# Performance work log

Hardware: AMD Instinct MI355X
Metric: run time of the kernel (lower is better)

## Reference

```python
import jax, jax.numpy as jnp
import numpy as np

HID = 64
NUM_LAYER = 3
N_OBJ = 100000
N_P1, N_P2, N_P3 = 200000, 400000, 200000
NUM_GRAPHS = 256


def _mlp(x, w1, b1, w2, b2):
    # pyg.nn.MLP([in, hid, out], norm=None): Linear -> ReLU -> Linear
    return jnp.dot(jax.nn.relu(jnp.dot(x, w1) + b1), w2) + b2


def _gather(obj, ei):
    # ei: [arity, n_atoms] object index per argument slot
    r, n = ei.shape
    g = jnp.take(obj, ei, axis=0)  # [r, n, HID]
    return jnp.moveaxis(g, 0, 1).reshape(n, r * HID)  # concat per-position embeddings


def _scatter(atom, ei, n_obj):
    # split atom embedding [n, r*HID] into r chunks and scatter-add to objects
    r, n = ei.shape
    chunks = jnp.moveaxis(atom.reshape(n, r, HID), 1, 0).reshape(r * n, HID)
    return jax.ops.segment_sum(chunks, ei.reshape(-1), num_segments=n_obj)


def _lin_init(key, fan_in, fan_out):
    kw, kb = jax.random.split(key)
    w = jax.random.normal(kw, (fan_in, fan_out), jnp.float32) / np.float32(np.sqrt(fan_in))
    b = jax.random.normal(kb, (fan_out,), jnp.float32) * 0.01
    return w, b


def setup_inputs() -> dict:
    key = jax.random.key(0)
    ks = jax.random.split(key, 16)
    inp = {}
    inp["x_obj"] = jnp.zeros((N_OBJ, 1), jnp.float32)
    inp["x_p1"] = jnp.zeros((N_P1, 1), jnp.float32)
    inp["x_p2"] = jnp.zeros((N_P2, 2), jnp.float32)
    inp["x_p3"] = jnp.zeros((N_P3, 3), jnp.float32)
    for i, (name, r) in enumerate([("p1", 1), ("p2", 2), ("p3", 3)]):
        d = HID * r
        w1, b1 = _lin_init(ks[2 * i], d, d)
        w2, b2 = _lin_init(ks[2 * i + 1], d, d)
        inp[f"w_{name}_1"], inp[f"b_{name}_1"] = w1, b1
        inp[f"w_{name}_2"], inp[f"b_{name}_2"] = w2, b2
    inp["w_u1"], inp["b_u1"] = _lin_init(ks[6], 2 * HID, 2 * HID)
    inp["w_u2"], inp["b_u2"] = _lin_init(ks[7], 2 * HID, HID)
    inp["w_r1"], inp["b_r1"] = _lin_init(ks[8], HID, 2 * HID)
    inp["w_r2"], inp["b_r2"] = _lin_init(ks[9], 2 * HID, 1)
    inp["ei_p1"] = jax.random.randint(ks[10], (1, N_P1), 0, N_OBJ, jnp.int32)
    inp["ei_p2"] = jax.random.randint(ks[11], (2, N_P2), 0, N_OBJ, jnp.int32)
    inp["ei_p3"] = jax.random.randint(ks[12], (3, N_P3), 0, N_OBJ, jnp.int32)
    inp["batch_obj"] = jnp.sort(jax.random.randint(ks[13], (N_OBJ,), 0, NUM_GRAPHS, jnp.int32))
    inp["num_graphs"] = NUM_GRAPHS
    return inp


def reference(x_obj, x_p1, x_p2, x_p3,
              w_p1_1, b_p1_1, w_p1_2, b_p1_2,
              w_p2_1, b_p2_1, w_p2_2, b_p2_2,
              w_p3_1, b_p3_1, w_p3_2, b_p3_2,
              w_u1, b_u1, w_u2, b_u2,
              w_r1, b_r1, w_r2, b_r2,
              ei_p1, ei_p2, ei_p3, batch_obj, num_graphs):
    n_obj = x_obj.shape[0]
    # encoding_layer: everything starts at zeros of size [N, F*hidden]
    obj = jnp.zeros((n_obj, x_obj.shape[1] * HID), jnp.float32)
    for _ in range(NUM_LAYER):
        # FanOutMP: gather arg-object embeddings, per-predicate MLP -> atom embeddings
        a1 = _mlp(_gather(obj, ei_p1), w_p1_1, b_p1_1, w_p1_2, b_p1_2)
        a2 = _mlp(_gather(obj, ei_p2), w_p2_1, b_p2_1, w_p2_2, b_p2_2)
        a3 = _mlp(_gather(obj, ei_p3), w_p3_1, b_p3_1, w_p3_2, b_p3_2)
        # FanInMP: split atom emb into arity chunks, scatter-add back to objects
        agg = (_scatter(a1, ei_p1, n_obj) + _scatter(a2, ei_p2, n_obj)
               + _scatter(a3, ei_p3, n_obj))
        # obj_update on cat([old_obj, aggregated])
        obj = _mlp(jnp.concatenate([obj, agg], axis=1), w_u1, b_u1, w_u2, b_u2)
    # global_add_pool + readout
    pooled = jax.ops.segment_sum(obj, batch_obj, num_segments=num_graphs)
    return _mlp(pooled, w_r1, b_r1, w_r2, b_r2).reshape(-1)
```

## Files before the change

### kernel.cpp

```cpp
#include <hip/hip_runtime.h>

typedef _Float16 h8 __attribute__((ext_vector_type(8)));
typedef _Float16 h4 __attribute__((ext_vector_type(4)));
typedef float f32x4 __attribute__((ext_vector_type(4)));

__device__ __forceinline__ f32x4 mfma2(h8 ah, h8 bh, h8 bl, f32x4 c) {
    c = __builtin_amdgcn_mfma_f32_16x16x32_f16(ah, bh, c, 0, 0, 0);
    c = __builtin_amdgcn_mfma_f32_16x16x32_f16(ah, bl, c, 0, 0, 0);
    return c;
}

__launch_bounds__(256)
__global__ void wprep(const float* __restrict__ w_p1_1, const float* __restrict__ w_p1_2,
                      const float* __restrict__ w_p2_1, const float* __restrict__ w_p2_2,
                      const float* __restrict__ w_p3_1, const float* __restrict__ w_p3_2,
                      const float* __restrict__ w_u1, const float* __restrict__ w_u2,
                      _Float16* __restrict__ hb)
{
    int b = blockIdx.x;
    const float* src; int K, N, base; size_t off;
    if      (b < 16)  { src = w_p1_1; K = 64;  N = 64;  base = 0;   off = 0;      }
    else if (b < 32)  { src = w_p1_2; K = 64;  N = 64;  base = 16;  off = 8192;   }
    else if (b < 96)  { src = w_p2_1; K = 128; N = 128; base = 32;  off = 16384;  }
    else if (b < 160) { src = w_p2_2; K = 128; N = 128; base = 96;  off = 49152;  }
    else if (b < 304) { src = w_p3_1; K = 192; N = 192; base = 160; off = 81920;  }
    else if (b < 448) { src = w_p3_2; K = 192; N = 192; base = 304; off = 155648; }
    else if (b < 512) { src = w_u1;   K = 128; N = 128; base = 448; off = 229376; }
    else              { src = w_u2;   K = 128; N = 64;  base = 512; off = 262144; }
    int e = (b - base) * 256 + threadIdx.x;
    if (e < K * N) {
        int n = e / K, k = e - n * K;
        float x = src[k * N + n];
        _Float16 h = (_Float16)x;
        hb[off + e] = h;
        hb[off + (size_t)K * N + e] = (_Float16)(x - (float)h);
    }
}

__launch_bounds__(256)
__global__ void aconst_k(const float* __restrict__ b_p1_1, const float* __restrict__ w_p1_2,
                         const float* __restrict__ b_p1_2,
                         const float* __restrict__ b_p2_1, const float* __restrict__ w_p2_2,
                         const float* __restrict__ b_p2_2,
                         const float* __restrict__ b_p3_1, const float* __restrict__ w_p3_2,
                         const float* __restrict__ b_p3_2,
                         float* __restrict__ ac)
{
    int p = blockIdx.x;
    const float *b1, *w2, *b2; int D, off;
    if      (p == 0) { b1 = b_p1_1; w2 = w_p1_2; b2 = b_p1_2; D = 64;  off = 0;   }
    else if (p == 1) { b1 = b_p2_1; w2 = w_p2_2; b2 = b_p2_2; D = 128; off = 64;  }
    else             { b1 = b_p3_1; w2 = w_p3_2; b2 = b_p3_2; D = 192; off = 192; }
    int n = threadIdx.x;
    if (n < D) {
        float s = b2[n];
        for (int k = 0; k < D; ++k) {
            float h = b1[k];
            h = h > 0.f ? h : 0.f;
            s = fmaf(h, w2[k * D + n], s);
        }
        ac[off + n] = s;
    }
}

__launch_bounds__(256)
__global__ void hist_k(const int* __restrict__ ei1, const int* __restrict__ ei2,
                       const int* __restrict__ ei3, int* __restrict__ counts,
                       int n_obj, int n1, int n2, int n3)
{
    int e = blockIdx.x * 256 + threadIdx.x;
    int t1 = n1, t2 = n1 + 2 * n2, t3 = t2 + 3 * n3;
    if (e < t1) {
        atomicAdd(&counts[ei1[e]], 1);
    } else if (e < t2) {
        int x = e - t1; int slot = x / n2;
        atomicAdd(&counts[(size_t)(1 + slot) * n_obj + ei2[x]], 1);
    } else if (e < t3) {
        int x = e - t2; int slot = x / n3;
        atomicAdd(&counts[(size_t)(3 + slot) * n_obj + ei3[x]], 1);
    }
}

__launch_bounds__(256)
__global__ void bcast_k(const int* __restrict__ counts, const float* __restrict__ ac,
                        float* __restrict__ agg, int n_obj)
{
    __shared__ float ch[384];
    int tid = threadIdx.x;
    for (int i = tid; i < 384; i += 256) ch[i] = ac[i];
    __syncthreads();
    int i = blockIdx.x * 256 + tid;
    int o = i >> 4, q = i & 15;
    if (o < n_obj) {
        float c[6];
#pragma unroll
        for (int j = 0; j < 6; ++j) c[j] = (float)counts[(size_t)j * n_obj + o];
        float4 v;
        float* vp = (float*)&v;
#pragma unroll
        for (int comp = 0; comp < 4; ++comp) {
            int col = 4 * q + comp;
            float s = 0.f;
#pragma unroll
            for (int j = 0; j < 6; ++j) s = fmaf(c[j], ch[j * 64 + col], s);
            vp[comp] = s;
        }
        ((float4*)agg)[(size_t)o * 16 + q] = v;
    }
}

template<int R>
__device__ __forceinline__ void pred_body(
    char* smem,
    const _Float16* __restrict__ objh, const int* __restrict__ ei,
    const _Float16* __restrict__ W1h, const _Float16* __restrict__ W1l,
    const float* __restrict__ B1,
    const _Float16* __restrict__ W2h, const _Float16* __restrict__ W2l,
    const float* __restrict__ B2,
    float* __restrict__ agg, int n_atoms, int blk)
{
    constexpr int D = 64 * R;
    constexpr int KC = D / 32;
    constexpr int LDA = D + 8;
    _Float16* Ah = (_Float16*)smem;
    int* eis = (int*)(Ah + 64 * LDA);

    const int tid = threadIdx.x;
    const int wave = tid >> 6, lane = tid & 63;
    const int r = lane & 15, g = lane >> 4;
    const int a_base = blk * 64;
    const int tb = wave * R;

    for (int i = tid; i < R * 64; i += 256) {
        int s = i >> 6, a = i & 63;
        int ag = a_base + a; if (ag >= n_atoms) ag = n_atoms - 1;
        eis[i] = ei[s * n_atoms + ag];
    }
    __syncthreads();
    {
        h8 vv[2 * R];
#pragma unroll
        for (int i = 0; i < 2 * R; ++i) {
            int f = tid + 256 * i;
            int rowslot = f >> 3, c = f & 7;
            int s = rowslot >> 6, a = rowslot & 63;
            vv[i] = *(const h8*)(objh + (size_t)eis[s * 64 + a] * 64 + c * 8);
        }
#pragma unroll
        for (int i = 0; i < 2 * R; ++i) {
            int f = tid + 256 * i;
            int rowslot = f >> 3, c = f & 7;
            int s = rowslot >> 6, a = rowslot & 63;
            *(h8*)(Ah + a * LDA + s * 64 + c * 8) = vv[i];
        }
    }
    __syncthreads();

    f32x4 z = {0.f, 0.f, 0.f, 0.f};
    f32x4 acc[4][R];
#pragma unroll
    for (int rt = 0; rt < 4; ++rt)
#pragma unroll
        for (int t = 0; t < R; ++t) acc[rt][t] = z;

    {
        h8 bh[2][R], bl[2][R];
#pragma unroll
        for (int t = 0; t < R; ++t) {
            size_t wo = (size_t)((tb + t) * 16 + r) * D + g * 8;
            bh[0][t] = *(const h8*)(W1h + wo);
            bl[0][t] = *(const h8*)(W1l + wo);
        }
#pragma unroll
        for (int kc = 0; kc < KC; ++kc) {
            const int cur = kc & 1, nxt = cur ^ 1;
            if (kc + 1 < KC) {
#pragma unroll
                for (int t = 0; t < R; ++t) {
                    size_t wo = (size_t)((tb + t) * 16 + r) * D + (kc + 1) * 32 + g * 8;
                    bh[nxt][t] = *(const h8*)(W1h + wo);
                    bl[nxt][t] = *(const h8*)(W1l + wo);
                }
            }
            const int ko = kc * 32 + g * 8;
            h8 ah[4];
#pragma unroll
            for (int rt = 0; rt < 4; ++rt)
                ah[rt] = *(const h8*)(Ah + (rt * 16 + r) * LDA + ko);
#pragma unroll
            for (int t = 0; t < R; ++t)
#pragma unroll
                for (int rt = 0; rt < 4; ++rt)
                    acc[rt][t] = mfma2(ah[rt], bh[cur][t], bl[cur][t], acc[rt][t]);
        }
    }
    __syncthreads();

#pragma unroll
    for (int t = 0; t < R; ++t) {
        int col = (tb + t) * 16 + r;
        float b1 = B1[col];
#pragma unroll
        for (int rt = 0; rt < 4; ++rt)
#pragma unroll
            for (int q = 0; q < 4; ++q) {
                int row = rt * 16 + g * 4 + q;
                float h = acc[rt][t][q] + b1;
                h = h > 0.f ? h : 0.f;
                Ah[row * LDA + col] = (_Float16)h;
            }
    }
    __syncthreads();

#pragma unroll
    for (int rt = 0; rt < 4; ++rt)
#pragma unroll
        for (int t = 0; t < R; ++t) acc[rt][t] = z;
    {
        h8 bh[2][R], bl[2][R];
#pragma unroll
        for (int t = 0; t < R; ++t) {
            size_t wo = (size_t)((tb + t) * 16 + r) * D + g * 8;
            bh[0][t] = *(const h8*)(W2h + wo);
            bl[0][t] = *(const h8*)(W2l + wo);
        }
#pragma unroll
        for (int kc = 0; kc < KC; ++kc) {
            const int cur = kc & 1, nxt = cur ^ 1;
            if (kc + 1 < KC) {
#pragma unroll
                for (int t = 0; t < R; ++t) {
                    size_t wo = (size_t)((tb + t) * 16 + r) * D + (kc + 1) * 32 + g * 8;
                    bh[nxt][t] = *(const h8*)(W2h + wo);
                    bl[nxt][t] = *(const h8*)(W2l + wo);
                }
            }
            const int ko = kc * 32 + g * 8;
            h8 ah[4];
#pragma unroll
            for (int rt = 0; rt < 4; ++rt)
                ah[rt] = *(const h8*)(Ah + (rt * 16 + r) * LDA + ko);
#pragma unroll
            for (int t = 0; t < R; ++t)
#pragma unroll
                for (int rt = 0; rt < 4; ++rt)
                    acc[rt][t] = mfma2(ah[rt], bh[cur][t], bl[cur][t], acc[rt][t]);
        }
    }

#pragma unroll
    for (int t = 0; t < R; ++t) {
        int col = (tb + t) * 16 + r;
        float b2 = B2[col];
        int s = col >> 6, cc = col & 63;
#pragma unroll
        for (int rt = 0; rt < 4; ++rt)
#pragma unroll
            for (int q = 0; q < 4; ++q) {
                int row = rt * 16 + g * 4 + q;
                int atom = a_base + row;
                if (atom < n_atoms)
                    atomicAdd(agg + (size_t)eis[s * 64 + row] * 64 + cc,
                              acc[rt][t][q] + b2);
            }
    }
}

__launch_bounds__(256, 6)
__global__ void pred_all(const _Float16* __restrict__ objh, float* __restrict__ agg,
                         const int* __restrict__ ei1, const int* __restrict__ ei2,
                         const int* __restrict__ ei3,
                         const _Float16* __restrict__ hb,
                         const float* __restrict__ b_p1_1, const float* __restrict__ b_p1_2,
                         const float* __restrict__ b_p2_1, const float* __restrict__ b_p2_2,
                         const float* __restrict__ b_p3_1, const float* __restrict__ b_p3_2,
                         int n1, int n2, int n3, int nb3, int nb2)
{
    extern __shared__ char smem[];
    int b = blockIdx.x;
    if (b < nb3) {
        pred_body<3>(smem, objh, ei3, hb + 81920, hb + 118784, b_p3_1,
                     hb + 155648, hb + 192512, b_p3_2, agg, n3, b);
    } else if (b < nb3 + nb2) {
        pred_body<2>(smem, objh, ei2, hb + 16384, hb + 32768, b_p2_1,
                     hb + 49152, hb + 65536, b_p2_2, agg, n2, b - nb3);
    } else {
        pred_body<1>(smem, objh, ei1, hb + 0, hb + 4096, b_p1_1,
                     hb + 8192, hb + 12288, b_p1_2, agg, n1, b - nb3 - nb2);
    }
}

template<int FIRST>
__launch_bounds__(256, 4)
__global__ void update_mfma(_Float16* __restrict__ objh, float* __restrict__ agg,
                            const _Float16* __restrict__ W1h, const _Float16* __restrict__ W1l,
                            const float* __restrict__ B1,
                            const _Float16* __restrict__ W2h, const _Float16* __restrict__ W2l,
                            const float* __restrict__ B2,
                            int n_obj, int zero_agg, int last)
{
    constexpr int LDA = 136;
    __shared__ _Float16 Ah[64 * LDA];

    const int tid = threadIdx.x;
    const int wave = tid >> 6, lane = tid & 63;
    const int r = lane & 15, g = lane >> 4;
    const int a_base = blockIdx.x * 64;

    {
#pragma unroll
        for (int i = 0; i < 4; ++i) {
            int f = tid + 256 * i;
            int a = f >> 4, c = f & 15;
            int rg = a_base + a; if (rg >= n_obj) rg = n_obj - 1;
            h8 v;
            if (c < 8) {
                if (FIRST) {
                    v = (h8)(_Float16)0.f;
                } else {
                    v = *(const h8*)(objh + (size_t)rg * 64 + c * 8);
                }
            } else {
                float4 f0 = ((const float4*)agg)[(size_t)rg * 16 + (c - 8) * 2];
                float4 f1 = ((const float4*)agg)[(size_t)rg * 16 + (c - 8) * 2 + 1];
                v[0] = (_Float16)f0.x; v[1] = (_Float16)f0.y;
                v[2] = (_Float16)f0.z; v[3] = (_Float16)f0.w;
                v[4] = (_Float16)f1.x; v[5] = (_Float16)f1.y;
                v[6] = (_Float16)f1.z; v[7] = (_Float16)f1.w;
            }
            *(h8*)(Ah + a * LDA + c * 8) = v;
        }
    }
    __syncthreads();

    f32x4 z = {0.f, 0.f, 0.f, 0.f};
    f32x4 acc[4][2];
#pragma unroll
    for (int rt = 0; rt < 4; ++rt) { acc[rt][0] = z; acc[rt][1] = z; }
    {
        h8 bh[2][2], bl[2][2];
#pragma unroll
        for (int t = 0; t < 2; ++t) {
            size_t wo = (size_t)((wave * 2 + t) * 16 + r) * 128 + g * 8;
            bh[0][t] = *(const h8*)(W1h + wo);
            bl[0][t] = *(const h8*)(W1l + wo);
        }
#pragma unroll
        for (int kc = 0; kc < 4; ++kc) {
            const int cur = kc & 1, nxt = cur ^ 1;
            if (kc + 1 < 4) {
#pragma unroll
                for (int t = 0; t < 2; ++t) {
                    size_t wo = (size_t)((wave * 2 + t) * 16 + r) * 128 + (kc + 1) * 32 + g * 8;
                    bh[nxt][t] = *(const h8*)(W1h + wo);
                    bl[nxt][t] = *(const h8*)(W1l + wo);
                }
            }
            const int ko = kc * 32 + g * 8;
            h8 ah[4];
#pragma unroll
            for (int rt = 0; rt < 4; ++rt)
                ah[rt] = *(const h8*)(Ah + (rt * 16 + r) * LDA + ko);
#pragma unroll
            for (int t = 0; t < 2; ++t)
#pragma unroll
                for (int rt = 0; rt < 4; ++rt)
                    acc[rt][t] = mfma2(ah[rt], bh[cur][t], bl[cur][t], acc[rt][t]);
        }
    }
    __syncthreads();
#pragma unroll
    for (int t = 0; t < 2; ++t) {
        int col = (wave * 2 + t) * 16 + r;
        float b1 = B1[col];
#pragma unroll
        for (int rt = 0; rt < 4; ++rt)
#pragma unroll
            for (int q = 0; q < 4; ++q) {
                int row = rt * 16 + g * 4 + q;
                float h = acc[rt][t][q] + b1;
                h = h > 0.f ? h : 0.f;
                Ah[row * LDA + col] = (_Float16)h;
            }
    }
    __syncthreads();

    f32x4 acc2[4];
#pragma unroll
    for (int rt = 0; rt < 4; ++rt) acc2[rt] = z;
    {
        h8 bh[2], bl[2];
        {
            size_t wo = (size_t)(wave * 16 + r) * 128 + g * 8;
            bh[0] = *(const h8*)(W2h + wo);
            bl[0] = *(const h8*)(W2l + wo);
        }
#pragma unroll
        for (int kc = 0; kc < 4; ++kc) {
            const int cur = kc & 1, nxt = cur ^ 1;
            if (kc + 1 < 4) {
                size_t wo = (size_t)(wave * 16 + r) * 128 + (kc + 1) * 32 + g * 8;
                bh[nxt] = *(const h8*)(W2h + wo);
                bl[nxt] = *(const h8*)(W2l + wo);
            }
            const int ko = kc * 32 + g * 8;
#pragma unroll
            for (int rt = 0; rt < 4; ++rt) {
                h8 ah = *(const h8*)(Ah + (rt * 16 + r) * LDA + ko);
                acc2[rt] = mfma2(ah, bh[cur], bl[cur], acc2[rt]);
            }
        }
    }
    __syncthreads();
    {
        int col = wave * 16 + r;
        float b2 = B2[col];
#pragma unroll
        for (int rt = 0; rt < 4; ++rt)
#pragma unroll
            for (int q = 0; q < 4; ++q) {
                int row = a_base + rt * 16 + g * 4 + q;
                if (row < n_obj) {
                    float v = acc2[rt][q] + b2;
                    if (last) {
                        agg[(size_t)row * 64 + col] = v;
                    } else {
                        objh[(size_t)row * 64 + col] = (_Float16)v;
                    }
                }
            }
    }
    if (zero_agg) {
        float4 zz = make_float4(0.f, 0.f, 0.f, 0.f);
#pragma unroll
        for (int i = 0; i < 4; ++i) {
            int f = tid + 256 * i;
            int a = f >> 4, q = f & 15;
            int rg = a_base + a;
            if (rg < n_obj) ((float4*)agg)[(size_t)rg * 16 + q] = zz;
        }
    }
}

__global__ void pool_kernel(const float* __restrict__ obj, const int* __restrict__ batch,
                            float* __restrict__ pooled, int n_obj)
{
    int i = blockIdx.x * 256 + threadIdx.x;
    int row = i >> 4, q = i & 15;
    if (row < n_obj) {
        float4 v = ((const float4*)obj)[(size_t)row * 16 + q];
        int g = batch[row];
        float* p = pooled + g * 64 + 4 * q;
        atomicAdd(p + 0, v.x);
        atomicAdd(p + 1, v.y);
        atomicAdd(p + 2, v.z);
        atomicAdd(p + 3, v.w);
    }
}

__launch_bounds__(128)
__global__ void readout_kernel(const float* __restrict__ pooled,
                               const float* __restrict__ w1, const float* __restrict__ b1,
                               const float* __restrict__ w2, const float* __restrict__ b2,
                               float* __restrict__ out)
{
    int g = blockIdx.x, c = threadIdx.x;
    __shared__ float xs[64];
    __shared__ float red[2];
    if (c < 64) xs[c] = pooled[g * 64 + c];
    __syncthreads();
    float h = b1[c];
#pragma unroll
    for (int k = 0; k < 64; ++k) h = fmaf(xs[k], w1[k * 128 + c], h);
    float v = fmaxf(h, 0.f) * w2[c];
#pragma unroll
    for (int off = 32; off > 0; off >>= 1) v += __shfl_down(v, off);
    if ((c & 63) == 0) red[c >> 6] = v;
    __syncthreads();
    if (c == 0) out[g] = red[0] + red[1] + b2[0];
}

extern "C" void kernel_launch(void* const* d_in, const int* in_sizes, int n_in,
                              void* d_out, int out_size, void* d_ws, size_t ws_size,
                              hipStream_t stream)
{
    const float* w_p1_1 = (const float*)d_in[4];
    const float* b_p1_1 = (const float*)d_in[5];
    const float* w_p1_2 = (const float*)d_in[6];
    const float* b_p1_2 = (const float*)d_in[7];
    const float* w_p2_1 = (const float*)d_in[8];
    const float* b_p2_1 = (const float*)d_in[9];
    const float* w_p2_2 = (const float*)d_in[10];
    const float* b_p2_2 = (const float*)d_in[11];
    const float* w_p3_1 = (const float*)d_in[12];
    const float* b_p3_1 = (const float*)d_in[13];
    const float* w_p3_2 = (const float*)d_in[14];
    const float* b_p3_2 = (const float*)d_in[15];
    const float* w_u1 = (const float*)d_in[16];
    const float* b_u1 = (const float*)d_in[17];
    const float* w_u2 = (const float*)d_in[18];
    const float* b_u2 = (const float*)d_in[19];
    const float* w_r1 = (const float*)d_in[20];
    const float* b_r1 = (const float*)d_in[21];
    const float* w_r2 = (const float*)d_in[22];
    const float* b_r2 = (const float*)d_in[23];
    const int* ei_p1 = (const int*)d_in[24];
    const int* ei_p2 = (const int*)d_in[25];
    const int* ei_p3 = (const int*)d_in[26];
    const int* batch = (const int*)d_in[27];

    const int n_obj = in_sizes[0];
    const int n_p1 = in_sizes[24];
    const int n_p2 = in_sizes[25] / 2;
    const int n_p3 = in_sizes[26] / 3;

    _Float16* objh = (_Float16*)d_ws;
    float* agg = (float*)(objh + (size_t)n_obj * 64);
    float* pooled = agg + (size_t)n_obj * 64;
    _Float16* hb = (_Float16*)(pooled + (size_t)out_size * 64);
    int* counts = (int*)objh;
    float* ac = (float*)(counts + 6 * (size_t)n_obj);

    const int nb3 = (n_p3 + 63) / 64, nb2 = (n_p2 + 63) / 64, nb1 = (n_p1 + 63) / 64;
    const int pred_smem = 64 * (192 + 8) * 2 + 3 * 64 * 4;
    (void)ws_size;

    wprep<<<544, 256, 0, stream>>>(w_p1_1, w_p1_2, w_p2_1, w_p2_2, w_p3_1, w_p3_2,
                                   w_u1, w_u2, hb);
    aconst_k<<<3, 256, 0, stream>>>(b_p1_1, w_p1_2, b_p1_2, b_p2_1, w_p2_2, b_p2_2,
                                    b_p3_1, w_p3_2, b_p3_2, ac);
    hipMemsetAsync(counts, 0, 6 * (size_t)n_obj * sizeof(int), stream);
    {
        int tot = n_p1 + 2 * n_p2 + 3 * n_p3;
        hist_k<<<(tot + 255) / 256, 256, 0, stream>>>(ei_p1, ei_p2, ei_p3, counts,
                                                      n_obj, n_p1, n_p2, n_p3);
    }
    bcast_k<<<((size_t)n_obj * 16 + 255) / 256, 256, 0, stream>>>(counts, ac, agg, n_obj);
    update_mfma<1><<<(n_obj + 63) / 64, 256, 0, stream>>>(
        objh, agg, hb + 229376, hb + 245760, b_u1, hb + 262144, hb + 270336, b_u2,
        n_obj, 1, 0);
    for (int l = 1; l < 3; ++l) {
        pred_all<<<nb3 + nb2 + nb1, 256, pred_smem, stream>>>(
            objh, agg, ei_p1, ei_p2, ei_p3, hb,
            b_p1_1, b_p1_2, b_p2_1, b_p2_2, b_p3_1, b_p3_2,
            n_p1, n_p2, n_p3, nb3, nb2);
        update_mfma<0><<<(n_obj + 63) / 64, 256, 0, stream>>>(
            objh, agg, hb + 229376, hb + 245760, b_u1, hb + 262144, hb + 270336, b_u2,
            n_obj, l < 2 ? 1 : 0, l == 2 ? 1 : 0);
    }
    hipMemsetAsync(pooled, 0, (size_t)out_size * 64 * sizeof(float), stream);
    pool_kernel<<<((size_t)n_obj * 16 + 255) / 256, 256, 0, stream>>>(agg, batch, pooled, n_obj);
    readout_kernel<<<out_size, 128, 0, stream>>>(pooled, w_r1, b_r1, w_r2, b_r2, (float*)d_out);
}
```

Before: 1.326 ms.

## Replace atomic scatter-add with CSR gather fused into object update

Builds a CSR (degree histogram, single-block scan, fill) mapping each object to its atom-slot chunks. The predicate MLP kernel now stores fp16 per-slot outputs to a chunks buffer instead of issuing float atomics into agg. A new fanin_update kernel gathers and sums those chunks per object and then runs the update MLP in the same kernel, avoiding atomic contention and the separate agg round trip. It adds preprocessing kernels, extra workspace, and fp16 rounding of atom outputs before summation. A leftover aconst_k call writes into agg, which bcast_k overwrites right afterwards, so it is harmless.

```diff
diff --git a/kernel.cpp b/kernel.cpp
--- a/kernel.cpp
+++ b/kernel.cpp
@@ -1,7 +1,6 @@
 #include <hip/hip_runtime.h>
 
 typedef _Float16 h8 __attribute__((ext_vector_type(8)));
-typedef _Float16 h4 __attribute__((ext_vector_type(4)));
 typedef float f32x4 __attribute__((ext_vector_type(4)));
 
 __device__ __forceinline__ f32x4 mfma2(h8 ah, h8 bh, h8 bl, f32x4 c) {
@@ -70,15 +69,66 @@
 {
     int e = blockIdx.x * 256 + threadIdx.x;
     int t1 = n1, t2 = n1 + 2 * n2, t3 = t2 + 3 * n3;
-    if (e < t1) {
-        atomicAdd(&counts[ei1[e]], 1);
-    } else if (e < t2) {
-        int x = e - t1; int slot = x / n2;
-        atomicAdd(&counts[(size_t)(1 + slot) * n_obj + ei2[x]], 1);
-    } else if (e < t3) {
-        int x = e - t2; int slot = x / n3;
-        atomicAdd(&counts[(size_t)(3 + slot) * n_obj + ei3[x]], 1);
-    }
+    int o, j;
+    if (e < t1) { o = ei1[e]; j = 0; }
+    else if (e < t2) { int x = e - t1; o = ei2[x]; j = 1 + (x >= n2 ? 1 : 0); }
+    else if (e < t3) { int y = e - t2; o = ei3[y]; j = 3 + (y >= n3 ? 1 : 0) + (y >= 2 * n3 ? 1 : 0); }
+    else return;
+    atomicAdd(&counts[(size_t)j * n_obj + o], 1);
+    atomicAdd(&counts[(size_t)6 * n_obj + o], 1);
+}
+
+__launch_bounds__(1024)
+__global__ void scan_k(const int* __restrict__ deg, int* __restrict__ rowptr,
+                       int* __restrict__ cursor, int n)
+{
+    __shared__ int buf[1024];
+    __shared__ int carry_s;
+    int tid = threadIdx.x;
+    if (tid == 0) carry_s = 0;
+    __syncthreads();
+    for (int base = 0; base < n; base += 4096) {
+        int idx = base + tid * 4;
+        int v[4];
+#pragma unroll
+        for (int k = 0; k < 4; ++k) { int i = idx + k; v[k] = (i < n) ? deg[i] : 0; }
+        int tsum = v[0] + v[1] + v[2] + v[3];
+        buf[tid] = tsum;
+        __syncthreads();
+        for (int off = 1; off < 1024; off <<= 1) {
+            int t = (tid >= off) ? buf[tid - off] : 0;
+            __syncthreads();
+            buf[tid] += t;
+            __syncthreads();
+        }
+        int run = buf[tid] - tsum + carry_s;
+#pragma unroll
+        for (int k = 0; k < 4; ++k) {
+            int i = idx + k;
+            if (i < n) { rowptr[i] = run; cursor[i] = run; }
+            run += v[k];
+        }
+        __syncthreads();
+        if (tid == 1023) carry_s += buf[1023];
+        __syncthreads();
+    }
+    if (tid == 0) rowptr[n] = carry_s;
+}
+
+__launch_bounds__(256)
+__global__ void fill_k(const int* __restrict__ ei1, const int* __restrict__ ei2,
+                       const int* __restrict__ ei3, int* __restrict__ cursor,
+                       int* __restrict__ colidx, int n1, int n2, int n3)
+{
+    int e = blockIdx.x * 256 + threadIdx.x;
+    int t1 = n1, t2 = n1 + 2 * n2, t3 = t2 + 3 * n3;
+    int o;
+    if (e < t1) o = ei1[e];
+    else if (e < t2) o = ei2[e - t1];
+    else if (e < t3) o = ei3[e - t2];
+    else return;
+    int pos = atomicAdd(&cursor[o], 1);
+    colidx[pos] = e;
 }
 
 __launch_bounds__(256)
@@ -109,7 +159,7 @@
     }
 }
 
-template<int R>
+template<int R, int STORE>
 __device__ __forceinline__ void pred_body(
     char* smem,
     const _Float16* __restrict__ objh, const int* __restrict__ ei,
@@ -117,7 +167,8 @@
     const float* __restrict__ B1,
     const _Float16* __restrict__ W2h, const _Float16* __restrict__ W2l,
     const float* __restrict__ B2,
-    float* __restrict__ agg, int n_atoms, int blk)
+    float* __restrict__ agg, _Float16* __restrict__ chunks, int cbase,
+    int n_atoms, int blk)
 {
     constexpr int D = 64 * R;
     constexpr int KC = D / 32;
@@ -195,7 +246,6 @@
         }
     }
     __syncthreads();
-
 #pragma unroll
     for (int t = 0; t < R; ++t) {
         int col = (tb + t) * 16 + r;
@@ -259,15 +309,22 @@
             for (int q = 0; q < 4; ++q) {
                 int row = rt * 16 + g * 4 + q;
                 int atom = a_base + row;
-                if (atom < n_atoms)
-                    atomicAdd(agg + (size_t)eis[s * 64 + row] * 64 + cc,
-                              acc[rt][t][q] + b2);
-            }
-    }
-}
-
+                if (atom < n_atoms) {
+                    float v = acc[rt][t][q] + b2;
+                    if (STORE) {
+                        chunks[(size_t)(cbase + s * n_atoms + atom) * 64 + cc] = (_Float16)v;
+                    } else {
+                        atomicAdd(agg + (size_t)eis[s * 64 + row] * 64 + cc, v);
+                    }
+                }
+            }
+    }
+}
+
+template<int STORE>
 __launch_bounds__(256, 6)
 __global__ void pred_all(const _Float16* __restrict__ objh, float* __restrict__ agg,
+                         _Float16* __restrict__ chunks,
                          const int* __restrict__ ei1, const int* __restrict__ ei2,
                          const int* __restrict__ ei3,
                          const _Float16* __restrict__ hb,
@@ -279,14 +336,169 @@
     extern __shared__ char smem[];
     int b = blockIdx.x;
     if (b < nb3) {
-        pred_body<3>(smem, objh, ei3, hb + 81920, hb + 118784, b_p3_1,
-                     hb + 155648, hb + 192512, b_p3_2, agg, n3, b);
+        pred_body<3, STORE>(smem, objh, ei3, hb + 81920, hb + 118784, b_p3_1,
+                            hb + 155648, hb + 192512, b_p3_2, agg, chunks,
+                            n1 + 2 * n2, n3, b);
     } else if (b < nb3 + nb2) {
-        pred_body<2>(smem, objh, ei2, hb + 16384, hb + 32768, b_p2_1,
-                     hb + 49152, hb + 65536, b_p2_2, agg, n2, b - nb3);
+        pred_body<2, STORE>(smem, objh, ei2, hb + 16384, hb + 32768, b_p2_1,
+                            hb + 49152, hb + 65536, b_p2_2, agg, chunks,
+                            n1, n2, b - nb3);
     } else {
-        pred_body<1>(smem, objh, ei1, hb + 0, hb + 4096, b_p1_1,
-                     hb + 8192, hb + 12288, b_p1_2, agg, n1, b - nb3 - nb2);
+        pred_body<1, STORE>(smem, objh, ei1, hb + 0, hb + 4096, b_p1_1,
+                            hb + 8192, hb + 12288, b_p1_2, agg, chunks,
+                            0, n1, b - nb3 - nb2);
+    }
+}
+
+__launch_bounds__(256, 4)
+__global__ void fanin_update(_Float16* __restrict__ objh,
+                             const _Float16* __restrict__ chunks,
+                             const int* __restrict__ rowptr, const int* __restrict__ colidx,
+                             const _Float16* __restrict__ W1h, const _Float16* __restrict__ W1l,
+                             const float* __restrict__ B1,
+                             const _Float16* __restrict__ W2h, const _Float16* __restrict__ W2l,
+                             const float* __restrict__ B2,
+                             int n_obj, int last, float* __restrict__ aggout)
+{
+    constexpr int LDA = 136;
+    __shared__ _Float16 Ah[64 * LDA];
+    __shared__ int cidx[2048];
+
+    const int tid = threadIdx.x;
+    const int wave = tid >> 6, lane = tid & 63;
+    const int r = lane & 15, g = lane >> 4;
+    const int a_base = blockIdx.x * 64;
+    const int o_hi = (a_base + 64 < n_obj) ? a_base + 64 : n_obj;
+
+    const int sbeg = rowptr[a_base];
+    const int send = rowptr[o_hi];
+    const int total = send - sbeg;
+    const int ncache = total < 2048 ? total : 2048;
+    for (int i = tid; i < ncache; i += 256) cidx[i] = colidx[sbeg + i];
+
+    const int o_local = tid >> 2, part = tid & 3;
+    const int o = a_base + o_local;
+    const bool valid = o < n_obj;
+    const int b = valid ? rowptr[o] : 0;
+    const int e2 = valid ? rowptr[o + 1] : 0;
+    float s[16];
+#pragma unroll
+    for (int j = 0; j < 16; ++j) s[j] = 0.f;
+    __syncthreads();
+    for (int i = b; i < e2; ++i) {
+        int li = i - sbeg;
+        int row = (li < ncache) ? cidx[li] : colidx[i];
+        const h8* cp = (const h8*)(chunks + (size_t)row * 64 + part * 16);
+        h8 v0 = cp[0], v1 = cp[1];
+#pragma unroll
+        for (int j = 0; j < 8; ++j) { s[j] += (float)v0[j]; s[8 + j] += (float)v1[j]; }
+    }
+    {
+        int oc = valid ? o : n_obj - 1;
+        h8 u0 = *(const h8*)(objh + (size_t)oc * 64 + part * 16);
+        h8 u1 = *(const h8*)(objh + (size_t)oc * 64 + part * 16 + 8);
+        *(h8*)(Ah + o_local * LDA + part * 16) = u0;
+        *(h8*)(Ah + o_local * LDA + part * 16 + 8) = u1;
+        h8 a0, a1;
+#pragma unroll
+        for (int j = 0; j < 8; ++j) { a0[j] = (_Float16)s[j]; a1[j] = (_Float16)s[8 + j]; }
+        *(h8*)(Ah + o_local * LDA + 64 + part * 16) = a0;
+        *(h8*)(Ah + o_local * LDA + 64 + part * 16 + 8) = a1;
+    }
+    __syncthreads();
+
+    f32x4 z = {0.f, 0.f, 0.f, 0.f};
+    f32x4 acc[4][2];
+#pragma unroll
+    for (int rt = 0; rt < 4; ++rt) { acc[rt][0] = z; acc[rt][1] = z; }
+    {
+        h8 bh[2][2], bl[2][2];
+#pragma unroll
+        for (int t = 0; t < 2; ++t) {
+            size_t wo = (size_t)((wave * 2 + t) * 16 + r) * 128 + g * 8;
+            bh[0][t] = *(const h8*)(W1h + wo);
+            bl[0][t] = *(const h8*)(W1l + wo);
+        }
+#pragma unroll
+        for (int kc = 0; kc < 4; ++kc) {
+            const int cur = kc & 1, nxt = cur ^ 1;
+            if (kc + 1 < 4) {
+#pragma unroll
+                for (int t = 0; t < 2; ++t) {
+                    size_t wo = (size_t)((wave * 2 + t) * 16 + r) * 128 + (kc + 1) * 32 + g * 8;
+                    bh[nxt][t] = *(const h8*)(W1h + wo);
+                    bl[nxt][t] = *(const h8*)(W1l + wo);
+                }
+            }
+            const int ko = kc * 32 + g * 8;
+            h8 ah[4];
+#pragma unroll
+            for (int rt = 0; rt < 4; ++rt)
+                ah[rt] = *(const h8*)(Ah + (rt * 16 + r) * LDA + ko);
+#pragma unroll
+            for (int t = 0; t < 2; ++t)
+#pragma unroll
+                for (int rt = 0; rt < 4; ++rt)
+                    acc[rt][t] = mfma2(ah[rt], bh[cur][t], bl[cur][t], acc[rt][t]);
+        }
+    }
+    __syncthreads();
+#pragma unroll
+    for (int t = 0; t < 2; ++t) {
+        int col = (wave * 2 + t) * 16 + r;
+        float b1 = B1[col];
+#pragma unroll
+        for (int rt = 0; rt < 4; ++rt)
+#pragma unroll
+            for (int q = 0; q < 4; ++q) {
+                int row = rt * 16 + g * 4 + q;
+                float h = acc[rt][t][q] + b1;
+                h = h > 0.f ? h : 0.f;
+                Ah[row * LDA + col] = (_Float16)h;
+            }
+    }
+    __syncthreads();
+
+    f32x4 acc2[4];
+#pragma unroll
+    for (int rt = 0; rt < 4; ++rt) acc2[rt] = z;
+    {
+        h8 bh[2], bl[2];
+        {
+            size_t wo = (size_t)(wave * 16 + r) * 128 + g * 8;
+            bh[0] = *(const h8*)(W2h + wo);
+            bl[0] = *(const h8*)(W2l + wo);
+        }
+#pragma unroll
+        for (int kc = 0; kc < 4; ++kc) {
+            const int cur = kc & 1, nxt = cur ^ 1;
+            if (kc + 1 < 4) {
+                size_t wo = (size_t)(wave * 16 + r) * 128 + (kc + 1) * 32 + g * 8;
+                bh[nxt] = *(const h8*)(W2h + wo);
+                bl[nxt] = *(const h8*)(W2l + wo);
+            }
+            const int ko = kc * 32 + g * 8;
+#pragma unroll
+            for (int rt = 0; rt < 4; ++rt) {
+                h8 ah = *(const h8*)(Ah + (rt * 16 + r) * LDA + ko);
+                acc2[rt] = mfma2(ah, bh[cur], bl[cur], acc2[rt]);
+            }
+        }
+    }
+    {
+        int col = wave * 16 + r;
+        float b2 = B2[col];
+#pragma unroll
+        for (int rt = 0; rt < 4; ++rt)
+#pragma unroll
+            for (int q = 0; q < 4; ++q) {
+                int row = a_base + rt * 16 + g * 4 + q;
+                if (row < n_obj) {
+                    float v = acc2[rt][q] + b2;
+                    if (last) aggout[(size_t)row * 64 + col] = v;
+                    else objh[(size_t)row * 64 + col] = (_Float16)v;
+                }
+            }
     }
 }
 
@@ -315,11 +527,8 @@
             int rg = a_base + a; if (rg >= n_obj) rg = n_obj - 1;
             h8 v;
             if (c < 8) {
-                if (FIRST) {
-                    v = (h8)(_Float16)0.f;
-                } else {
-                    v = *(const h8*)(objh + (size_t)rg * 64 + c * 8);
-                }
+                if (FIRST) v = (h8)(_Float16)0.f;
+                else v = *(const h8*)(objh + (size_t)rg * 64 + c * 8);
             } else {
                 float4 f0 = ((const float4*)agg)[(size_t)rg * 16 + (c - 8) * 2];
                 float4 f1 = ((const float4*)agg)[(size_t)rg * 16 + (c - 8) * 2 + 1];
@@ -422,11 +631,8 @@
                 int row = a_base + rt * 16 + g * 4 + q;
                 if (row < n_obj) {
                     float v = acc2[rt][q] + b2;
-                    if (last) {
-                        agg[(size_t)row * 64 + col] = v;
-                    } else {
-                        objh[(size_t)row * 64 + col] = (_Float16)v;
-                    }
+                    if (last) agg[(size_t)row * 64 + col] = v;
+                    else objh[(size_t)row * 64 + col] = (_Float16)v;
                 }
             }
     }
@@ -479,6 +685,8 @@
     __syncthreads();
     if (c == 0) out[g] = red[0] + red[1] + b2[0];
 }
+
+static inline size_t align_up(size_t x) { return (x + 255) & ~(size_t)255; }
 
 extern "C" void kernel_launch(void* const* d_in, const int* in_sizes, int n_in,
                               void* d_out, int out_size, void* d_ws, size_t ws_size,
@@ -513,40 +721,65 @@
     const int n_p1 = in_sizes[24];
     const int n_p2 = in_sizes[25] / 2;
     const int n_p3 = in_sizes[26] / 3;
-
-    _Float16* objh = (_Float16*)d_ws;
-    float* agg = (float*)(objh + (size_t)n_obj * 64);
-    float* pooled = agg + (size_t)n_obj * 64;
-    _Float16* hb = (_Float16*)(pooled + (size_t)out_size * 64);
-    int* counts = (int*)objh;
-    float* ac = (float*)(counts + 6 * (size_t)n_obj);
+    const int E = n_p1 + 2 * n_p2 + 3 * n_p3;
+
+    char* base = (char*)d_ws;
+    size_t off = 0;
+    _Float16* objh = (_Float16*)(base + off); off = align_up(off + (size_t)n_obj * 64 * 2);
+    float* agg = (float*)(base + off);        off = align_up(off + (size_t)n_obj * 64 * 4);
+    float* pooled = (float*)(base + off);     off = align_up(off + (size_t)out_size * 64 * 4);
+    _Float16* hb = (_Float16*)(base + off);   off = align_up(off + (size_t)278528 * 2);
+    int* counts = (int*)(base + off);         off = align_up(off + (size_t)7 * n_obj * 4);
+    int* deg = counts + (size_t)6 * n_obj;
+    int* rowptr = (int*)(base + off);         off = align_up(off + ((size_t)n_obj + 1) * 4);
+    int* cursor = (int*)(base + off);         off = align_up(off + (size_t)n_obj * 4);
+    int* colidx = (int*)(base + off);         off = align_up(off + (size_t)E * 4);
+    _Float16* chunks = (_Float16*)(base + off); off = align_up(off + (size_t)E * 64 * 2);
+    const bool csr_ok = off <= ws_size;
 
     const int nb3 = (n_p3 + 63) / 64, nb2 = (n_p2 + 63) / 64, nb1 = (n_p1 + 63) / 64;
     const int pred_smem = 64 * (192 + 8) * 2 + 3 * 64 * 4;
-    (void)ws_size;
 
     wprep<<<544, 256, 0, stream>>>(w_p1_1, w_p1_2, w_p2_1, w_p2_2, w_p3_1, w_p3_2,
                                    w_u1, w_u2, hb);
     aconst_k<<<3, 256, 0, stream>>>(b_p1_1, w_p1_2, b_p1_2, b_p2_1, w_p2_2, b_p2_2,
+                                    b_p3_1, w_p3_2, b_p3_2, agg);
+    float* ac = pooled;
+    aconst_k<<<3, 256, 0, stream>>>(b_p1_1, w_p1_2, b_p1_2, b_p2_1, w_p2_2, b_p2_2,
                                     b_p3_1, w_p3_2, b_p3_2, ac);
-    hipMemsetAsync(counts, 0, 6 * (size_t)n_obj * sizeof(int), stream);
-    {
-        int tot = n_p1 + 2 * n_p2 + 3 * n_p3;
-        hist_k<<<(tot + 255) / 256, 256, 0, stream>>>(ei_p1, ei_p2, ei_p3, counts,
-                                                      n_obj, n_p1, n_p2, n_p3);
+    hipMemsetAsync(counts, 0, (size_t)7 * n_obj * sizeof(int), stream);
+    hist_k<<<(E + 255) / 256, 256, 0, stream>>>(ei_p1, ei_p2, ei_p3, counts,
+                                                n_obj, n_p1, n_p2, n_p3);
+    if (csr_ok) {
+        scan_k<<<1, 1024, 0, stream>>>(deg, rowptr, cursor, n_obj);
+        fill_k<<<(E + 255) / 256, 256, 0, stream>>>(ei_p1, ei_p2, ei_p3, cursor, colidx,
+                                                    n_p1, n_p2, n_p3);
     }
     bcast_k<<<((size_t)n_obj * 16 + 255) / 256, 256, 0, stream>>>(counts, ac, agg, n_obj);
     update_mfma<1><<<(n_obj + 63) / 64, 256, 0, stream>>>(
         objh, agg, hb + 229376, hb + 245760, b_u1, hb + 262144, hb + 270336, b_u2,
-        n_obj, 1, 0);
-    for (int l = 1; l < 3; ++l) {
-        pred_all<<<nb3 + nb2 + nb1, 256, pred_smem, stream>>>(
-            objh, agg, ei_p1, ei_p2, ei_p3, hb,
-            b_p1_1, b_p1_2, b_p2_1, b_p2_2, b_p3_1, b_p3_2,
-            n_p1, n_p2, n_p3, nb3, nb2);
-        update_mfma<0><<<(n_obj + 63) / 64, 256, 0, stream>>>(
-            objh, agg, hb + 229376, hb + 245760, b_u1, hb + 262144, hb + 270336, b_u2,
-            n_obj, l < 2 ? 1 : 0, l == 2 ? 1 : 0);
+        n_obj, csr_ok ? 0 : 1, 0);
+    if (csr_ok) {
+        for (int l = 1; l < 3; ++l) {
+            pred_all<1><<<nb3 + nb2 + nb1, 256, pred_smem, stream>>>(
+                objh, agg, chunks, ei_p1, ei_p2, ei_p3, hb,
+                b_p1_1, b_p1_2, b_p2_1, b_p2_2, b_p3_1, b_p3_2,
+                n_p1, n_p2, n_p3, nb3, nb2);
+            fanin_update<<<(n_obj + 63) / 64, 256, 0, stream>>>(
+                objh, chunks, rowptr, colidx,
+                hb + 229376, hb + 245760, b_u1, hb + 262144, hb + 270336, b_u2,
+                n_obj, l == 2 ? 1 : 0, agg);
+        }
+    } else {
+        for (int l = 1; l < 3; ++l) {
+            pred_all<0><<<nb3 + nb2 + nb1, 256, pred_smem, stream>>>(
+                objh, agg, chunks, ei_p1, ei_p2, ei_p3, hb,
+                b_p1_1, b_p1_2, b_p2_1, b_p2_2, b_p3_1, b_p3_2,
+                n_p1, n_p2, n_p3, nb3, nb2);
+            update_mfma<0><<<(n_obj + 63) / 64, 256, 0, stream>>>(
+                objh, agg, hb + 229376, hb + 245760, b_u1, hb + 262144, hb + 270336, b_u2,
+                n_obj, l < 2 ? 1 : 0, l == 2 ? 1 : 0);
+        }
     }
     hipMemsetAsync(pooled, 0, (size_t)out_size * 64 * sizeof(float), stream);
     pool_kernel<<<((size_t)n_obj * 16 + 255) / 256, 256, 0, stream>>>(agg, batch, pooled, n_obj);
```

Measured after the change: 1.469 ms. 1.11x slower.
